# Kernel tuning notes

Hardware: AMD Instinct MI355X
Metric: run time of the kernel (lower is better)

Reference implementation:

```python
import jax, jax.numpy as jnp
import numpy as np

L, E, H, V = 12, 1024, 4096, 50277
LN_EPS = 9.999999747378752e-06  # tf float32 1e-5


def _layernorm(x, w, b):
    m = jnp.mean(x)
    xc = x - m
    return xc / jnp.sqrt(jnp.mean(xc * xc) + LN_EPS) * w + b


def setup_inputs() -> dict:
    key = jax.random.key(0)
    ks = jax.random.split(key, 32)
    f32 = jnp.float32

    def n(i, shape, s=0.02):
        return (jax.random.normal(ks[i], shape, f32) * s).astype(f32)

    inp = {
        "statea": n(0, (L, E), 0.3),
        "stateb": jax.random.uniform(ks[1], (L, E), f32),
        "statec": jax.random.uniform(ks[2], (L, E), f32),
        "stated": n(3, (L, E), 0.3),
        "preprocess": n(4, (V, E), 0.5),
        "ln1w": 1.0 + n(5, (L, E), 0.05),
        "ln1b": n(6, (L, E), 0.05),
        "ln2w": 1.0 + n(7, (L, E), 0.05),
        "ln2b": n(8, (L, E), 0.05),
        "att_key": n(9, (L, E, E)),
        "att_receptance": n(10, (L, E, E)),
        "att_value": n(11, (L, E, E)),
        "kktk": jax.random.uniform(ks[12], (L, E), f32),
        "vvtv": jax.random.uniform(ks[13], (L, E), f32),
        "rrtr": jax.random.uniform(ks[14], (L, E), f32),
        "time_first": n(15, (L, E), 0.2),
        "time_decay": n(16, (L, E), 0.2) - 1.0,
        "outputvv": n(17, (L, E, E)),
        "time_mix_k_ffn": jax.random.uniform(ks[18], (L, E), f32),
        "time_mix_r_ffn": jax.random.uniform(ks[19], (L, E), f32),
        "key_ffn": n(20, (L, H, E)),
        "receptance_ffn": n(21, (L, E, E)),
        "value_ffn": n(22, (L, E, H)),
        "post0": 1.0 + n(23, (E,), 0.05),
        "post1": n(24, (E,), 0.05),
        "post2": n(25, (V, E)),
        "token": 123,
    }
    return inp


def _forward(statea, stateb, statec, stated, preprocess, ln1w, ln1b, ln2w, ln2b,
             att_key, att_receptance, att_value, kktk, vvtv, rrtr, time_first,
             time_decay, outputvv, time_mix_k_ffn, time_mix_r_ffn, key_ffn,
             receptance_ffn, value_ffn, post0, post1, post2, token):
    x0 = preprocess[token]  # [E]

    def step(x, p):
        (sa, sb, sc, sd, l1w, l1b, l2w, l2b, ak, ar, av, kk, vv, rr,
         tfirst, tdecay, ovv, tmk_m, tmr_m, kf, rf, vf) = p
        xy = _layernorm(x, l1w, l1b)
        # WKV time-mixing (single step): mat-vecs + exp-decay state recursion
        k = jnp.exp(ak @ (xy + kk * sa))        # [E]
        v = av @ (xy + vv * sa)                 # [E]
        r = jnp.exp(ar @ (xy + rr * sa)) + 1.0  # [E]
        etf = jnp.exp(tfirst)
        w = sb + etf * k * v
        d = sc * r + etf * k * r
        mvv = ovv @ (w / (d + 0.001))           # [E]
        sxx = x + mvv
        aaa = xy
        etd = jnp.exp(tdecay)
        bbb = sb * etd + k * v
        ccc = sc * etd + k
        # channel-mixing FFN
        xx = _layernorm(sxx, l2w, l2b)
        kma = kf @ (xx + tmk_m * sd)            # [H]
        km = jnp.square(jnp.maximum(kma, 0.0))
        rt = jnp.exp(rf @ (xx + tmr_m * sd)) + 1.0  # [E]
        x_new = sxx + (vf @ km) / rt
        ddd = xx
        return x_new, (aaa, bbb, ccc, ddd)

    xs = (statea, stateb, statec, stated, ln1w, ln1b, ln2w, ln2b, att_key,
          att_receptance, att_value, kktk, vvtv, rrtr, time_first, time_decay,
          outputvv, time_mix_k_ffn, time_mix_r_ffn, key_ffn, receptance_ffn,
          value_ffn)
    xL, (aaa, bbb, ccc, ddd) = jax.lax.scan(step, x0, xs)
    logits = post2 @ _layernorm(xL, post0, post1)  # [V]
    return logits, aaa, bbb, ccc, ddd


def reference(statea, stateb, statec, stated, preprocess, ln1w, ln1b, ln2w, ln2b,
              att_key, att_receptance, att_value, kktk, vvtv, rrtr, time_first,
              time_decay, outputvv, time_mix_k_ffn, time_mix_r_ffn, key_ffn,
              receptance_ffn, value_ffn, post0, post1, post2, token):
    return _forward(statea, stateb, statec, stated, preprocess, ln1w, ln1b,
                    ln2w, ln2b, att_key, att_receptance, att_value, kktk, vvtv,
                    rrtr, time_first, time_decay, outputvv, time_mix_k_ffn,
                    time_mix_r_ffn, key_ffn, receptance_ffn, value_ffn, post0,
                    post1, post2, token)
```

## Files before the change

### kernel.cpp

```cpp
#include <hip/hip_runtime.h>
#include <math.h>


constexpr int E = 1024;
constexpr int H = 4096;
constexpr int V = 50277;
constexpr int L = 12;
constexpr int NBLK = 256;
constexpr int NTHR = 512;
constexpr float LN_EPS = 9.999999747378752e-06f;

#define SCOPE_AGENT __HIP_MEMORY_SCOPE_AGENT

__device__ __forceinline__ void cstoref(float *p, float v) {
  __hip_atomic_store(p, v, __ATOMIC_RELAXED, SCOPE_AGENT);
}
__device__ __forceinline__ void cstoreu(unsigned *p, unsigned v) {
  __hip_atomic_store(p, v, __ATOMIC_RELAXED, SCOPE_AGENT);
}
__device__ __forceinline__ unsigned cloadu(const unsigned *p) {
  return __hip_atomic_load(p, __ATOMIC_RELAXED, SCOPE_AGENT);
}

__device__ __forceinline__ float2 cload2(const void *p) {
  float2 r;
  asm volatile("global_load_dwordx2 %0, %1, off sc0 sc1\n\t"
               "s_waitcnt vmcnt(0)"
               : "=&v"(r) : "v"(p) : "memory");
  return r;
}
__device__ __forceinline__ void cload4x2(float4 &r0, float4 &r1,
                                         const void *p0, const void *p1) {
  asm volatile("global_load_dwordx4 %0, %2, off sc0 sc1\n\t"
               "global_load_dwordx4 %1, %3, off sc0 sc1\n\t"
               "s_waitcnt vmcnt(0)"
               : "=&v"(r0), "=&v"(r1) : "v"(p0), "v"(p1) : "memory");
}

struct Args {
  const float *statea, *stateb, *statec, *stated, *pre;
  const float *ln1w, *ln1b, *ln2w, *ln2b;
  const float *ak, *ar, *av, *kk, *vv, *rr, *tf, *td, *ovv;
  const float *tmk, *tmr, *kf, *rf, *vf;
  const float *post0, *post1, *post2;
  const int *token;
  float *out;
  float *ws;
  unsigned *flags;
};

__device__ __forceinline__ void bar_arrive(const Args &a, unsigned ep, int blk) {
  __syncthreads();
  if (threadIdx.x == 0) cstoreu(&a.flags[blk * 32], ep);
}

__device__ __forceinline__ void bar_wait(const Args &a, unsigned ep) {
  if (threadIdx.x < NBLK) {
    while (cloadu(&a.flags[threadIdx.x * 32]) < ep)
      __builtin_amdgcn_s_sleep(2);
  }
  __syncthreads();
}

__device__ __forceinline__ float wred(float v) {
#pragma unroll
  for (int off = 32; off; off >>= 1) v += __shfl_down(v, off, 64);
  return v;
}

__device__ __forceinline__ float dot4(float4 w, float4 x) {
  return w.x * x.x + w.y * x.y + w.z * x.z + w.w * x.w;
}

__device__ __forceinline__ float2 block_stats_v(float2 v, float *s_x, float *s_red,
                                                int tid, int lane, int wid) {
  reinterpret_cast<float2 *>(s_x)[tid] = v;
  float s = v.x + v.y, s2 = v.x * v.x + v.y * v.y;
#pragma unroll
  for (int off = 32; off; off >>= 1) {
    s += __shfl_down(s, off, 64);
    s2 += __shfl_down(s2, off, 64);
  }
  if (lane == 0) { s_red[wid] = s; s_red[8 + wid] = s2; }
  __syncthreads();
  float ts = 0.f, ts2 = 0.f;
#pragma unroll
  for (int i = 0; i < 8; ++i) { ts += s_red[i]; ts2 += s_red[8 + i]; }
  float m = ts * (1.0f / E);
  float var = ts2 * (1.0f / E) - m * m;
  return make_float2(m, rsqrtf(var + LN_EPS));
}

__device__ __forceinline__ void loadrow(float4 *d, const float4 *P, int r, int lane) {
  const float4 *p = P + (size_t)r * 256;
  d[0] = p[lane]; d[1] = p[lane + 64]; d[2] = p[lane + 128]; d[3] = p[lane + 192];
}

__global__ __launch_bounds__(NTHR) void rwkv_fused(Args a) {
  __shared__ __align__(16) float s_a[4096];
  __shared__ __align__(16) float s_x[1024];
  __shared__ __align__(16) float s_y[1024];
  __shared__ float s_pp[24];
  __shared__ float s_red[16];
  __shared__ float s_rt[4];

  const int tid = threadIdx.x;
  const int lane = tid & 63;
  const int wid = tid >> 6;
  const int blk = blockIdx.x;
  const int rloc = wid >> 1;
  const int h = wid & 1;
  const int grow = blk * 4 + rloc;

  float *ws_u = a.ws, *ws_sxx = a.ws + 1024, *ws_x = a.ws + 2048, *ws_km = a.ws + 3072;
  float *out_logits = a.out;
  float *out_aaa = a.out + V;
  float *out_bbb = out_aaa + L * E;
  float *out_ccc = out_bbb + L * E;
  float *out_ddd = out_ccc + L * E;

  const int tok = a.token[0];
  const float *pre_row = a.pre + (size_t)tok * E;
  const float4 *s4a = reinterpret_cast<const float4 *>(s_a);

  float4 pw[10];
  unsigned ep = 1;

  {
    const float4 *kr = reinterpret_cast<const float4 *>(a.ak + (size_t)grow * E);
    const float4 *vr = reinterpret_cast<const float4 *>(a.av + (size_t)grow * E);
    const float4 *rr = reinterpret_cast<const float4 *>(a.ar + (size_t)grow * E);
    int b0 = h * 128 + lane;
    pw[0] = kr[b0]; pw[1] = kr[b0 + 64];
    pw[2] = vr[b0]; pw[3] = vr[b0 + 64];
    pw[4] = rr[b0]; pw[5] = rr[b0 + 64];
    asm volatile("" ::: "memory");
  }

  for (int l = 0; l < L; ++l) {
    const size_t lE = (size_t)l * E;

    {
      float2 v;
      if (l == 0) {
        v = reinterpret_cast<const float2 *>(pre_row)[tid];
      } else {
        v = cload2(reinterpret_cast<const float2 *>(ws_x) + tid);
      }
      float2 st = block_stats_v(v, s_x, s_red, tid, lane, wid);
#pragma unroll
      for (int j = 0; j < 2; ++j) {
        int e = tid + 512 * j;
        float xy = (s_x[e] - st.x) * st.y * a.ln1w[lE + e] + a.ln1b[lE + e];
        s_y[e] = xy;
        float sa = a.statea[lE + e];
        s_a[e] = xy + a.kk[lE + e] * sa;
        s_a[1024 + e] = xy + a.vv[lE + e] * sa;
        s_a[2048 + e] = xy + a.rr[lE + e] * sa;
      }
      __syncthreads();
      int b0 = h * 128 + lane;
      float accK = dot4(pw[0], s4a[b0]) + dot4(pw[1], s4a[b0 + 64]);
      float accV = dot4(pw[2], s4a[256 + b0]) + dot4(pw[3], s4a[256 + b0 + 64]);
      float accR = dot4(pw[4], s4a[512 + b0]) + dot4(pw[5], s4a[512 + b0 + 64]);
      accK = wred(accK); accV = wred(accV); accR = wred(accR);
      if (lane == 0) {
        s_pp[wid * 3 + 0] = accK;
        s_pp[wid * 3 + 1] = accV;
        s_pp[wid * 3 + 2] = accR;
      }
      __syncthreads();
      if (tid < 4) {
        size_t o = lE + blk * 4 + tid;
        float K = s_pp[(2 * tid) * 3] + s_pp[(2 * tid + 1) * 3];
        float Vv = s_pp[(2 * tid) * 3 + 1] + s_pp[(2 * tid + 1) * 3 + 1];
        float R = s_pp[(2 * tid) * 3 + 2] + s_pp[(2 * tid + 1) * 3 + 2];
        float kx = expf(K), rx = expf(R) + 1.0f;
        float etf = expf(a.tf[o]), etd = expf(a.td[o]);
        float sb = a.stateb[o], sc = a.statec[o];
        float w_ = sb + etf * kx * Vv;
        float d_ = sc * rx + etf * kx * rx;
        cstoref(&ws_u[blk * 4 + tid], w_ / (d_ + 0.001f));
        out_bbb[o] = sb * etd + kx * Vv;
        out_ccc[o] = sc * etd + kx;
        out_aaa[o] = s_y[blk * 4 + tid];
      }
    }
    bar_arrive(a, ep, blk);
    {
      const float4 *orow = reinterpret_cast<const float4 *>(a.ovv + (lE + grow) * E);
      int b0 = h * 128 + lane;
      pw[0] = orow[b0]; pw[1] = orow[b0 + 64];
      asm volatile("" ::: "memory");
    }
    bar_wait(a, ep); ++ep;

    {
      reinterpret_cast<float2 *>(s_a)[tid] =
          cload2(reinterpret_cast<const float2 *>(ws_u) + tid);
      __syncthreads();
      int b0 = h * 128 + lane;
      float acc = dot4(pw[0], s4a[b0]) + dot4(pw[1], s4a[b0 + 64]);
      acc = wred(acc);
      if (lane == 0) s_pp[wid] = acc;
      __syncthreads();
      if (tid < 4) {
        float sxx = s_x[blk * 4 + tid] + s_pp[2 * tid] + s_pp[2 * tid + 1];
        cstoref(&ws_sxx[blk * 4 + tid], sxx);
      }
    }
    bar_arrive(a, ep, blk);
    {
      const float *kfb = a.kf + (size_t)l * H * E;
      const float4 *k0 = reinterpret_cast<const float4 *>(kfb + (size_t)(blk * 16 + wid) * E);
      const float4 *k1 = reinterpret_cast<const float4 *>(kfb + (size_t)(blk * 16 + 8 + wid) * E);
      pw[0] = k0[lane];       pw[1] = k0[lane + 64];
      pw[2] = k0[lane + 128]; pw[3] = k0[lane + 192];
      pw[4] = k1[lane];       pw[5] = k1[lane + 64];
      pw[6] = k1[lane + 128]; pw[7] = k1[lane + 192];
      const float4 *rrow = reinterpret_cast<const float4 *>(a.rf + (lE + grow) * E);
      int b0 = h * 128 + lane;
      pw[8] = rrow[b0]; pw[9] = rrow[b0 + 64];
      asm volatile("" ::: "memory");
    }
    bar_wait(a, ep); ++ep;

    {
      float2 v = cload2(reinterpret_cast<const float2 *>(ws_sxx) + tid);
      float2 st = block_stats_v(v, s_x, s_red, tid, lane, wid);
#pragma unroll
      for (int j = 0; j < 2; ++j) {
        int e = tid + 512 * j;
        float xx = (s_x[e] - st.x) * st.y * a.ln2w[lE + e] + a.ln2b[lE + e];
        s_y[e] = xx;
        float sd = a.stated[lE + e];
        s_a[e] = xx + a.tmk[lE + e] * sd;
        s_a[1024 + e] = xx + a.tmr[lE + e] * sd;
      }
      __syncthreads();
      float k0 = dot4(pw[0], s4a[lane]) + dot4(pw[1], s4a[lane + 64]) +
                 dot4(pw[2], s4a[lane + 128]) + dot4(pw[3], s4a[lane + 192]);
      float k1 = dot4(pw[4], s4a[lane]) + dot4(pw[5], s4a[lane + 64]) +
                 dot4(pw[6], s4a[lane + 128]) + dot4(pw[7], s4a[lane + 192]);
      int b0 = h * 128 + lane;
      float ar_ = dot4(pw[8], s4a[256 + b0]) + dot4(pw[9], s4a[256 + b0 + 64]);
      k0 = wred(k0); k1 = wred(k1); ar_ = wred(ar_);
      if (lane == 0) {
        float t0 = fmaxf(k0, 0.f), t1 = fmaxf(k1, 0.f);
        cstoref(&ws_km[blk * 16 + wid], t0 * t0);
        cstoref(&ws_km[blk * 16 + 8 + wid], t1 * t1);
        s_pp[wid] = ar_;
      }
      __syncthreads();
      if (tid < 4) {
        s_rt[tid] = expf(s_pp[2 * tid] + s_pp[2 * tid + 1]) + 1.0f;
        out_ddd[lE + blk * 4 + tid] = s_y[blk * 4 + tid];
      }
    }
    bar_arrive(a, ep, blk);
    {
      const float4 *vrow = reinterpret_cast<const float4 *>(a.vf + (lE + grow) * H);
      int b0 = h * 512 + lane;
      pw[0] = vrow[b0];       pw[1] = vrow[b0 + 64];
      pw[2] = vrow[b0 + 128]; pw[3] = vrow[b0 + 192];
      pw[4] = vrow[b0 + 256]; pw[5] = vrow[b0 + 320];
      pw[6] = vrow[b0 + 384]; pw[7] = vrow[b0 + 448];
      asm volatile("" ::: "memory");
    }
    bar_wait(a, ep); ++ep;

    {
      float4 km0, km1;
      cload4x2(km0, km1,
               reinterpret_cast<const float4 *>(ws_km) + tid,
               reinterpret_cast<const float4 *>(ws_km) + tid + 512);
      reinterpret_cast<float4 *>(s_a)[tid] = km0;
      reinterpret_cast<float4 *>(s_a)[tid + 512] = km1;
      __syncthreads();
      int b0 = h * 512 + lane;
      float acc = dot4(pw[0], s4a[b0]) + dot4(pw[1], s4a[b0 + 64]) +
                  dot4(pw[2], s4a[b0 + 128]) + dot4(pw[3], s4a[b0 + 192]) +
                  dot4(pw[4], s4a[b0 + 256]) + dot4(pw[5], s4a[b0 + 320]) +
                  dot4(pw[6], s4a[b0 + 384]) + dot4(pw[7], s4a[b0 + 448]);
      acc = wred(acc);
      if (lane == 0) s_pp[wid] = acc;
      __syncthreads();
      if (tid < 4) {
        float xn = s_x[blk * 4 + tid] + (s_pp[2 * tid] + s_pp[2 * tid + 1]) / s_rt[tid];
        cstoref(&ws_x[blk * 4 + tid], xn);
      }
    }
    bar_arrive(a, ep, blk);
    if (l < L - 1) {
      const size_t lE2 = (size_t)(l + 1) * E;
      const float4 *kr = reinterpret_cast<const float4 *>(a.ak + (lE2 + grow) * E);
      const float4 *vr = reinterpret_cast<const float4 *>(a.av + (lE2 + grow) * E);
      const float4 *rr = reinterpret_cast<const float4 *>(a.ar + (lE2 + grow) * E);
      int b0 = h * 128 + lane;
      pw[0] = kr[b0]; pw[1] = kr[b0 + 64];
      pw[2] = vr[b0]; pw[3] = vr[b0 + 64];
      pw[4] = rr[b0]; pw[5] = rr[b0 + 64];
      asm volatile("" ::: "memory");
    }
    bar_wait(a, ep); ++ep;
  }

  {
    float2 v = cload2(reinterpret_cast<const float2 *>(ws_x) + tid);
    float2 st = block_stats_v(v, s_x, s_red, tid, lane, wid);
#pragma unroll
    for (int j = 0; j < 2; ++j) {
      int e = tid + 512 * j;
      s_a[e] = (s_x[e] - st.x) * st.y * a.post0[e] + a.post1[e];
    }
    __syncthreads();

    const float4 *P2 = reinterpret_cast<const float4 *>(a.post2);
    const int gw = blk * 8 + wid;
    int r0 = gw, r1 = gw + 2048;
    float4 A0[4], A1[4];
    loadrow(A0, P2, r0, lane);
    loadrow(A1, P2, r1 < V ? r1 : r0, lane);
    while (true) {
      int n0 = r0 + 4096, n1 = n0 + 2048;
      bool more = n0 < V;
      float4 B0[4], B1[4];
      if (more) {
        loadrow(B0, P2, n0, lane);
        loadrow(B1, P2, n1 < V ? n1 : n0, lane);
      }
      float a0 = dot4(A0[0], s4a[lane]) + dot4(A0[1], s4a[lane + 64]) +
                 dot4(A0[2], s4a[lane + 128]) + dot4(A0[3], s4a[lane + 192]);
      float a1 = dot4(A1[0], s4a[lane]) + dot4(A1[1], s4a[lane + 64]) +
                 dot4(A1[2], s4a[lane + 128]) + dot4(A1[3], s4a[lane + 192]);
      a0 = wred(a0); a1 = wred(a1);
      if (lane == 0) {
        out_logits[r0] = a0;
        if (r1 < V) out_logits[r1] = a1;
      }
      if (!more) break;
#pragma unroll
      for (int q = 0; q < 4; ++q) { A0[q] = B0[q]; A1[q] = B1[q]; }
      r0 = n0; r1 = n1;
    }
  }
}

extern "C" void kernel_launch(void *const *d_in, const int *in_sizes, int n_in,
                              void *d_out, int out_size, void *d_ws, size_t ws_size,
                              hipStream_t stream) {
  (void)in_sizes; (void)n_in; (void)out_size; (void)ws_size;
  Args a;
  a.statea = (const float *)d_in[0];
  a.stateb = (const float *)d_in[1];
  a.statec = (const float *)d_in[2];
  a.stated = (const float *)d_in[3];
  a.pre    = (const float *)d_in[4];
  a.ln1w   = (const float *)d_in[5];
  a.ln1b   = (const float *)d_in[6];
  a.ln2w   = (const float *)d_in[7];
  a.ln2b   = (const float *)d_in[8];
  a.ak     = (const float *)d_in[9];
  a.ar     = (const float *)d_in[10];
  a.av     = (const float *)d_in[11];
  a.kk     = (const float *)d_in[12];
  a.vv     = (const float *)d_in[13];
  a.rr     = (const float *)d_in[14];
  a.tf     = (const float *)d_in[15];
  a.td     = (const float *)d_in[16];
  a.ovv    = (const float *)d_in[17];
  a.tmk    = (const float *)d_in[18];
  a.tmr    = (const float *)d_in[19];
  a.kf     = (const float *)d_in[20];
  a.rf     = (const float *)d_in[21];
  a.vf     = (const float *)d_in[22];
  a.post0  = (const float *)d_in[23];
  a.post1  = (const float *)d_in[24];
  a.post2  = (const float *)d_in[25];
  a.token  = (const int *)d_in[26];
  a.out    = (float *)d_out;

  a.flags  = (unsigned *)d_ws;
  a.ws     = (float *)((char *)d_ws + 32768);

  hipMemsetAsync(d_ws, 0, 32768, stream);
  rwkv_fused<<<NBLK, NTHR, 0, stream>>>(a);
}
```

Baseline: 242.4 us.

## Prefetch weights stages ahead and replace syncthreads with lighter LDS barriers

Measured after the change: 266.8 us. 10.1% more time.

```diff
diff --git a/kernel.cpp b/kernel.cpp
--- a/kernel.cpp
+++ b/kernel.cpp
@@ -21,20 +21,17 @@
 __device__ __forceinline__ unsigned cloadu(const unsigned *p) {
   return __hip_atomic_load(p, __ATOMIC_RELAXED, SCOPE_AGENT);
 }
-
-__device__ __forceinline__ float2 cload2(const void *p) {
-  float2 r;
-  asm volatile("global_load_dwordx2 %0, %1, off sc0 sc1\n\t"
-               "s_waitcnt vmcnt(0)"
-               : "=&v"(r) : "v"(p) : "memory");
-  return r;
-}
-__device__ __forceinline__ void cload4x2(float4 &r0, float4 &r1,
-                                         const void *p0, const void *p1) {
-  asm volatile("global_load_dwordx4 %0, %2, off sc0 sc1\n\t"
-               "global_load_dwordx4 %1, %3, off sc0 sc1\n\t"
-               "s_waitcnt vmcnt(0)"
-               : "=&v"(r0), "=&v"(r1) : "v"(p0), "v"(p1) : "memory");
+__device__ __forceinline__ float2 cload2(const float *p) {
+  union { unsigned long long u; float2 f; } c;
+  c.u = __hip_atomic_load((const unsigned long long *)p, __ATOMIC_RELAXED, SCOPE_AGENT);
+  return c.f;
+}
+
+__device__ __forceinline__ void lds_sync() {
+  __builtin_amdgcn_sched_barrier(0);
+  asm volatile("s_waitcnt lgkmcnt(0)" ::: "memory");
+  __builtin_amdgcn_s_barrier();
+  __builtin_amdgcn_sched_barrier(0);
 }
 
 struct Args {
@@ -52,14 +49,17 @@
 __device__ __forceinline__ void bar_arrive(const Args &a, unsigned ep, int blk) {
   __syncthreads();
   if (threadIdx.x == 0) cstoreu(&a.flags[blk * 32], ep);
-}
-
-__device__ __forceinline__ void bar_wait(const Args &a, unsigned ep) {
+  __builtin_amdgcn_sched_barrier(0);
+}
+
+__device__ __forceinline__ void bar_spin(const Args &a, unsigned ep) {
+  __builtin_amdgcn_sched_barrier(0);
   if (threadIdx.x < NBLK) {
     while (cloadu(&a.flags[threadIdx.x * 32]) < ep)
       __builtin_amdgcn_s_sleep(2);
   }
-  __syncthreads();
+  __builtin_amdgcn_s_barrier();
+  __builtin_amdgcn_sched_barrier(0);
 }
 
 __device__ __forceinline__ float wred(float v) {
@@ -82,7 +82,7 @@
     s2 += __shfl_down(s2, off, 64);
   }
   if (lane == 0) { s_red[wid] = s; s_red[8 + wid] = s2; }
-  __syncthreads();
+  lds_sync();
   float ts = 0.f, ts2 = 0.f;
 #pragma unroll
   for (int i = 0; i < 8; ++i) { ts += s_red[i]; ts2 += s_red[8 + i]; }
@@ -111,6 +111,8 @@
   const int rloc = wid >> 1;
   const int h = wid & 1;
   const int grow = blk * 4 + rloc;
+  const int b0h = h * 128 + lane;
+  const int bv = h * 512 + lane;
 
   float *ws_u = a.ws, *ws_sxx = a.ws + 1024, *ws_x = a.ws + 2048, *ws_km = a.ws + 3072;
   float *out_logits = a.out;
@@ -123,87 +125,114 @@
   const float *pre_row = a.pre + (size_t)tok * E;
   const float4 *s4a = reinterpret_cast<const float4 *>(s_a);
 
-  float4 pw[10];
   unsigned ep = 1;
+
+  float4 pw1[6];
+  float2 e1w, e1b, e1sa, e1kk, e1vv, e1rr;
+  float e_tf = 0.f, e_td = 0.f, e_sb = 0.f, e_sc = 0.f;
 
   {
     const float4 *kr = reinterpret_cast<const float4 *>(a.ak + (size_t)grow * E);
     const float4 *vr = reinterpret_cast<const float4 *>(a.av + (size_t)grow * E);
-    const float4 *rr = reinterpret_cast<const float4 *>(a.ar + (size_t)grow * E);
-    int b0 = h * 128 + lane;
-    pw[0] = kr[b0]; pw[1] = kr[b0 + 64];
-    pw[2] = vr[b0]; pw[3] = vr[b0 + 64];
-    pw[4] = rr[b0]; pw[5] = rr[b0 + 64];
-    asm volatile("" ::: "memory");
+    const float4 *rr4 = reinterpret_cast<const float4 *>(a.ar + (size_t)grow * E);
+    pw1[0] = kr[b0h]; pw1[1] = kr[b0h + 64];
+    pw1[2] = vr[b0h]; pw1[3] = vr[b0h + 64];
+    pw1[4] = rr4[b0h]; pw1[5] = rr4[b0h + 64];
+    e1w = reinterpret_cast<const float2 *>(a.ln1w)[tid];
+    e1b = reinterpret_cast<const float2 *>(a.ln1b)[tid];
+    e1sa = reinterpret_cast<const float2 *>(a.statea)[tid];
+    e1kk = reinterpret_cast<const float2 *>(a.kk)[tid];
+    e1vv = reinterpret_cast<const float2 *>(a.vv)[tid];
+    e1rr = reinterpret_cast<const float2 *>(a.rr)[tid];
+    if (tid < 4) {
+      size_t o = (size_t)blk * 4 + tid;
+      e_tf = a.tf[o]; e_td = a.td[o]; e_sb = a.stateb[o]; e_sc = a.statec[o];
+    }
   }
 
+#pragma unroll 1
   for (int l = 0; l < L; ++l) {
     const size_t lE = (size_t)l * E;
+    float4 pw2[2], pw3[10], pw4[8];
+    float2 e3w, e3b, e3sd, e3tk, e3tr;
 
     {
       float2 v;
-      if (l == 0) {
-        v = reinterpret_cast<const float2 *>(pre_row)[tid];
-      } else {
-        v = cload2(reinterpret_cast<const float2 *>(ws_x) + tid);
+      if (l == 0) v = reinterpret_cast<const float2 *>(pre_row)[tid];
+      else        v = cload2(ws_x + 2 * tid);
+      {
+        const float4 *orow = reinterpret_cast<const float4 *>(a.ovv + (lE + grow) * E);
+        pw2[0] = orow[b0h]; pw2[1] = orow[b0h + 64];
+        const float *kfb = a.kf + (size_t)l * H * E;
+        const float4 *k0 = reinterpret_cast<const float4 *>(kfb + (size_t)(blk * 16 + wid) * E);
+        pw3[0] = k0[lane];       pw3[1] = k0[lane + 64];
+        pw3[2] = k0[lane + 128]; pw3[3] = k0[lane + 192];
       }
       float2 st = block_stats_v(v, s_x, s_red, tid, lane, wid);
-#pragma unroll
-      for (int j = 0; j < 2; ++j) {
-        int e = tid + 512 * j;
-        float xy = (s_x[e] - st.x) * st.y * a.ln1w[lE + e] + a.ln1b[lE + e];
-        s_y[e] = xy;
-        float sa = a.statea[lE + e];
-        s_a[e] = xy + a.kk[lE + e] * sa;
-        s_a[1024 + e] = xy + a.vv[lE + e] * sa;
-        s_a[2048 + e] = xy + a.rr[lE + e] * sa;
-      }
-      __syncthreads();
-      int b0 = h * 128 + lane;
-      float accK = dot4(pw[0], s4a[b0]) + dot4(pw[1], s4a[b0 + 64]);
-      float accV = dot4(pw[2], s4a[256 + b0]) + dot4(pw[3], s4a[256 + b0 + 64]);
-      float accR = dot4(pw[4], s4a[512 + b0]) + dot4(pw[5], s4a[512 + b0 + 64]);
+      float2 xy = make_float2((v.x - st.x) * st.y * e1w.x + e1b.x,
+                              (v.y - st.x) * st.y * e1w.y + e1b.y);
+      reinterpret_cast<float2 *>(s_y)[tid] = xy;
+      reinterpret_cast<float2 *>(s_a)[tid] =
+          make_float2(xy.x + e1kk.x * e1sa.x, xy.y + e1kk.y * e1sa.y);
+      reinterpret_cast<float2 *>(s_a + 1024)[tid] =
+          make_float2(xy.x + e1vv.x * e1sa.x, xy.y + e1vv.y * e1sa.y);
+      reinterpret_cast<float2 *>(s_a + 2048)[tid] =
+          make_float2(xy.x + e1rr.x * e1sa.x, xy.y + e1rr.y * e1sa.y);
+      lds_sync();
+      float accK = dot4(pw1[0], s4a[b0h]) + dot4(pw1[1], s4a[b0h + 64]);
+      float accV = dot4(pw1[2], s4a[256 + b0h]) + dot4(pw1[3], s4a[256 + b0h + 64]);
+      float accR = dot4(pw1[4], s4a[512 + b0h]) + dot4(pw1[5], s4a[512 + b0h + 64]);
       accK = wred(accK); accV = wred(accV); accR = wred(accR);
       if (lane == 0) {
         s_pp[wid * 3 + 0] = accK;
         s_pp[wid * 3 + 1] = accV;
         s_pp[wid * 3 + 2] = accR;
       }
-      __syncthreads();
+      lds_sync();
       if (tid < 4) {
         size_t o = lE + blk * 4 + tid;
         float K = s_pp[(2 * tid) * 3] + s_pp[(2 * tid + 1) * 3];
         float Vv = s_pp[(2 * tid) * 3 + 1] + s_pp[(2 * tid + 1) * 3 + 1];
         float R = s_pp[(2 * tid) * 3 + 2] + s_pp[(2 * tid + 1) * 3 + 2];
         float kx = expf(K), rx = expf(R) + 1.0f;
-        float etf = expf(a.tf[o]), etd = expf(a.td[o]);
-        float sb = a.stateb[o], sc = a.statec[o];
-        float w_ = sb + etf * kx * Vv;
-        float d_ = sc * rx + etf * kx * rx;
+        float etf = expf(e_tf), etd = expf(e_td);
+        float w_ = e_sb + etf * kx * Vv;
+        float d_ = e_sc * rx + etf * kx * rx;
         cstoref(&ws_u[blk * 4 + tid], w_ / (d_ + 0.001f));
-        out_bbb[o] = sb * etd + kx * Vv;
-        out_ccc[o] = sc * etd + kx;
+        out_bbb[o] = e_sb * etd + kx * Vv;
+        out_ccc[o] = e_sc * etd + kx;
         out_aaa[o] = s_y[blk * 4 + tid];
       }
     }
     bar_arrive(a, ep, blk);
     {
-      const float4 *orow = reinterpret_cast<const float4 *>(a.ovv + (lE + grow) * E);
-      int b0 = h * 128 + lane;
-      pw[0] = orow[b0]; pw[1] = orow[b0 + 64];
-      asm volatile("" ::: "memory");
-    }
-    bar_wait(a, ep); ++ep;
-
-    {
-      reinterpret_cast<float2 *>(s_a)[tid] =
-          cload2(reinterpret_cast<const float2 *>(ws_u) + tid);
-      __syncthreads();
-      int b0 = h * 128 + lane;
-      float acc = dot4(pw[0], s4a[b0]) + dot4(pw[1], s4a[b0 + 64]);
+      const float *kfb = a.kf + (size_t)l * H * E;
+      const float4 *k1 = reinterpret_cast<const float4 *>(kfb + (size_t)(blk * 16 + 8 + wid) * E);
+      pw3[4] = k1[lane];       pw3[5] = k1[lane + 64];
+      pw3[6] = k1[lane + 128]; pw3[7] = k1[lane + 192];
+    }
+    bar_spin(a, ep); ++ep;
+
+    {
+      float2 u2 = cload2(ws_u + 2 * tid);
+      {
+        const float4 *rrow = reinterpret_cast<const float4 *>(a.rf + (lE + grow) * E);
+        pw3[8] = rrow[b0h]; pw3[9] = rrow[b0h + 64];
+        e3w = reinterpret_cast<const float2 *>(a.ln2w + lE)[tid];
+        e3b = reinterpret_cast<const float2 *>(a.ln2b + lE)[tid];
+        e3sd = reinterpret_cast<const float2 *>(a.stated + lE)[tid];
+        e3tk = reinterpret_cast<const float2 *>(a.tmk + lE)[tid];
+        e3tr = reinterpret_cast<const float2 *>(a.tmr + lE)[tid];
+        const float4 *vrow = reinterpret_cast<const float4 *>(a.vf + (lE + grow) * H);
+        pw4[0] = vrow[bv];       pw4[1] = vrow[bv + 64];
+        pw4[2] = vrow[bv + 128]; pw4[3] = vrow[bv + 192];
+      }
+      reinterpret_cast<float2 *>(s_a)[tid] = u2;
+      lds_sync();
+      float acc = dot4(pw2[0], s4a[b0h]) + dot4(pw2[1], s4a[b0h + 64]);
       acc = wred(acc);
       if (lane == 0) s_pp[wid] = acc;
-      __syncthreads();
+      lds_sync();
       if (tid < 4) {
         float sxx = s_x[blk * 4 + tid] + s_pp[2 * tid] + s_pp[2 * tid + 1];
         cstoref(&ws_sxx[blk * 4 + tid], sxx);
@@ -211,109 +240,99 @@
     }
     bar_arrive(a, ep, blk);
     {
-      const float *kfb = a.kf + (size_t)l * H * E;
-      const float4 *k0 = reinterpret_cast<const float4 *>(kfb + (size_t)(blk * 16 + wid) * E);
-      const float4 *k1 = reinterpret_cast<const float4 *>(kfb + (size_t)(blk * 16 + 8 + wid) * E);
-      pw[0] = k0[lane];       pw[1] = k0[lane + 64];
-      pw[2] = k0[lane + 128]; pw[3] = k0[lane + 192];
-      pw[4] = k1[lane];       pw[5] = k1[lane + 64];
-      pw[6] = k1[lane + 128]; pw[7] = k1[lane + 192];
-      const float4 *rrow = reinterpret_cast<const float4 *>(a.rf + (lE + grow) * E);
-      int b0 = h * 128 + lane;
-      pw[8] = rrow[b0]; pw[9] = rrow[b0 + 64];
-      asm volatile("" ::: "memory");
-    }
-    bar_wait(a, ep); ++ep;
-
-    {
-      float2 v = cload2(reinterpret_cast<const float2 *>(ws_sxx) + tid);
-      float2 st = block_stats_v(v, s_x, s_red, tid, lane, wid);
-#pragma unroll
-      for (int j = 0; j < 2; ++j) {
-        int e = tid + 512 * j;
-        float xx = (s_x[e] - st.x) * st.y * a.ln2w[lE + e] + a.ln2b[lE + e];
-        s_y[e] = xx;
-        float sd = a.stated[lE + e];
-        s_a[e] = xx + a.tmk[lE + e] * sd;
-        s_a[1024 + e] = xx + a.tmr[lE + e] * sd;
-      }
-      __syncthreads();
-      float k0 = dot4(pw[0], s4a[lane]) + dot4(pw[1], s4a[lane + 64]) +
-                 dot4(pw[2], s4a[lane + 128]) + dot4(pw[3], s4a[lane + 192]);
-      float k1 = dot4(pw[4], s4a[lane]) + dot4(pw[5], s4a[lane + 64]) +
-                 dot4(pw[6], s4a[lane + 128]) + dot4(pw[7], s4a[lane + 192]);
-      int b0 = h * 128 + lane;
-      float ar_ = dot4(pw[8], s4a[256 + b0]) + dot4(pw[9], s4a[256 + b0 + 64]);
+      const float4 *vrow = reinterpret_cast<const float4 *>(a.vf + (lE + grow) * H);
+      pw4[4] = vrow[bv + 256]; pw4[5] = vrow[bv + 320];
+      pw4[6] = vrow[bv + 384]; pw4[7] = vrow[bv + 448];
+    }
+    bar_spin(a, ep); ++ep;
+
+    {
+      float2 vsx = cload2(ws_sxx + 2 * tid);
+      if (l + 1 < L) {
+        const size_t nE = (size_t)(l + 1) * E;
+        const float4 *kr = reinterpret_cast<const float4 *>(a.ak + (nE + grow) * E);
+        const float4 *vr = reinterpret_cast<const float4 *>(a.av + (nE + grow) * E);
+        const float4 *rr4 = reinterpret_cast<const float4 *>(a.ar + (nE + grow) * E);
+        pw1[0] = kr[b0h]; pw1[1] = kr[b0h + 64];
+        pw1[2] = vr[b0h]; pw1[3] = vr[b0h + 64];
+        pw1[4] = rr4[b0h]; pw1[5] = rr4[b0h + 64];
+        e1w = reinterpret_cast<const float2 *>(a.ln1w + nE)[tid];
+        e1b = reinterpret_cast<const float2 *>(a.ln1b + nE)[tid];
+        e1sa = reinterpret_cast<const float2 *>(a.statea + nE)[tid];
+        e1kk = reinterpret_cast<const float2 *>(a.kk + nE)[tid];
+        e1vv = reinterpret_cast<const float2 *>(a.vv + nE)[tid];
+        e1rr = reinterpret_cast<const float2 *>(a.rr + nE)[tid];
+        if (tid < 4) {
+          size_t o = nE + blk * 4 + tid;
+          e_tf = a.tf[o]; e_td = a.td[o]; e_sb = a.stateb[o]; e_sc = a.statec[o];
+        }
+      } else {
+        e1w = reinterpret_cast<const float2 *>(a.post0)[tid];
+        e1b = reinterpret_cast<const float2 *>(a.post1)[tid];
+      }
+      float2 st = block_stats_v(vsx, s_x, s_red, tid, lane, wid);
+      float2 xx = make_float2((vsx.x - st.x) * st.y * e3w.x + e3b.x,
+                              (vsx.y - st.x) * st.y * e3w.y + e3b.y);
+      reinterpret_cast<float2 *>(s_y)[tid] = xx;
+      reinterpret_cast<float2 *>(s_a)[tid] =
+          make_float2(xx.x + e3tk.x * e3sd.x, xx.y + e3tk.y * e3sd.y);
+      reinterpret_cast<float2 *>(s_a + 1024)[tid] =
+          make_float2(xx.x + e3tr.x * e3sd.x, xx.y + e3tr.y * e3sd.y);
+      lds_sync();
+      float k0 = dot4(pw3[0], s4a[lane]) + dot4(pw3[1], s4a[lane + 64]) +
+                 dot4(pw3[2], s4a[lane + 128]) + dot4(pw3[3], s4a[lane + 192]);
+      float k1 = dot4(pw3[4], s4a[lane]) + dot4(pw3[5], s4a[lane + 64]) +
+                 dot4(pw3[6], s4a[lane + 128]) + dot4(pw3[7], s4a[lane + 192]);
+      float ar_ = dot4(pw3[8], s4a[256 + b0h]) + dot4(pw3[9], s4a[256 + b0h + 64]);
       k0 = wred(k0); k1 = wred(k1); ar_ = wred(ar_);
       if (lane == 0) {
-        float t0 = fmaxf(k0, 0.f), t1 = fmaxf(k1, 0.f);
+        float t0 = fmaxf(k0, 0.f), t1v = fmaxf(k1, 0.f);
         cstoref(&ws_km[blk * 16 + wid], t0 * t0);
-        cstoref(&ws_km[blk * 16 + 8 + wid], t1 * t1);
+        cstoref(&ws_km[blk * 16 + 8 + wid], t1v * t1v);
         s_pp[wid] = ar_;
       }
-      __syncthreads();
+      lds_sync();
       if (tid < 4) {
         s_rt[tid] = expf(s_pp[2 * tid] + s_pp[2 * tid + 1]) + 1.0f;
         out_ddd[lE + blk * 4 + tid] = s_y[blk * 4 + tid];
       }
     }
     bar_arrive(a, ep, blk);
-    {
-      const float4 *vrow = reinterpret_cast<const float4 *>(a.vf + (lE + grow) * H);
-      int b0 = h * 512 + lane;
-      pw[0] = vrow[b0];       pw[1] = vrow[b0 + 64];
-      pw[2] = vrow[b0 + 128]; pw[3] = vrow[b0 + 192];
-      pw[4] = vrow[b0 + 256]; pw[5] = vrow[b0 + 320];
-      pw[6] = vrow[b0 + 384]; pw[7] = vrow[b0 + 448];
-      asm volatile("" ::: "memory");
-    }
-    bar_wait(a, ep); ++ep;
-
-    {
-      float4 km0, km1;
-      cload4x2(km0, km1,
-               reinterpret_cast<const float4 *>(ws_km) + tid,
-               reinterpret_cast<const float4 *>(ws_km) + tid + 512);
-      reinterpret_cast<float4 *>(s_a)[tid] = km0;
-      reinterpret_cast<float4 *>(s_a)[tid + 512] = km1;
-      __syncthreads();
-      int b0 = h * 512 + lane;
-      float acc = dot4(pw[0], s4a[b0]) + dot4(pw[1], s4a[b0 + 64]) +
-                  dot4(pw[2], s4a[b0 + 128]) + dot4(pw[3], s4a[b0 + 192]) +
-                  dot4(pw[4], s4a[b0 + 256]) + dot4(pw[5], s4a[b0 + 320]) +
-                  dot4(pw[6], s4a[b0 + 384]) + dot4(pw[7], s4a[b0 + 448]);
+    bar_spin(a, ep); ++ep;
+
+    {
+      float2 k0a = cload2(ws_km + 4 * tid);
+      float2 k0b = cload2(ws_km + 4 * tid + 2);
+      float2 k1a = cload2(ws_km + 2048 + 4 * tid);
+      float2 k1b = cload2(ws_km + 2048 + 4 * tid + 2);
+      reinterpret_cast<float2 *>(s_a)[2 * tid] = k0a;
+      reinterpret_cast<float2 *>(s_a)[2 * tid + 1] = k0b;
+      reinterpret_cast<float2 *>(s_a)[1024 + 2 * tid] = k1a;
+      reinterpret_cast<float2 *>(s_a)[1024 + 2 * tid + 1] = k1b;
+      lds_sync();
+      float acc = dot4(pw4[0], s4a[bv]) + dot4(pw4[1], s4a[bv + 64]) +
+                  dot4(pw4[2], s4a[bv + 128]) + dot4(pw4[3], s4a[bv + 192]) +
+                  dot4(pw4[4], s4a[bv + 256]) + dot4(pw4[5], s4a[bv + 320]) +
+                  dot4(pw4[6], s4a[bv + 384]) + dot4(pw4[7], s4a[bv + 448]);
       acc = wred(acc);
       if (lane == 0) s_pp[wid] = acc;
-      __syncthreads();
+      lds_sync();
       if (tid < 4) {
         float xn = s_x[blk * 4 + tid] + (s_pp[2 * tid] + s_pp[2 * tid + 1]) / s_rt[tid];
         cstoref(&ws_x[blk * 4 + tid], xn);
       }
     }
     bar_arrive(a, ep, blk);
-    if (l < L - 1) {
-      const size_t lE2 = (size_t)(l + 1) * E;
-      const float4 *kr = reinterpret_cast<const float4 *>(a.ak + (lE2 + grow) * E);
-      const float4 *vr = reinterpret_cast<const float4 *>(a.av + (lE2 + grow) * E);
-      const float4 *rr = reinterpret_cast<const float4 *>(a.ar + (lE2 + grow) * E);
-      int b0 = h * 128 + lane;
-      pw[0] = kr[b0]; pw[1] = kr[b0 + 64];
-      pw[2] = vr[b0]; pw[3] = vr[b0 + 64];
-      pw[4] = rr[b0]; pw[5] = rr[b0 + 64];
-      asm volatile("" ::: "memory");
-    }
-    bar_wait(a, ep); ++ep;
+    bar_spin(a, ep); ++ep;
   }
 
   {
-    float2 v = cload2(reinterpret_cast<const float2 *>(ws_x) + tid);
+    float2 v = cload2(ws_x + 2 * tid);
     float2 st = block_stats_v(v, s_x, s_red, tid, lane, wid);
-#pragma unroll
-    for (int j = 0; j < 2; ++j) {
-      int e = tid + 512 * j;
-      s_a[e] = (s_x[e] - st.x) * st.y * a.post0[e] + a.post1[e];
-    }
-    __syncthreads();
+    reinterpret_cast<float2 *>(s_a)[tid] =
+        make_float2((v.x - st.x) * st.y * e1w.x + e1b.x,
+                    (v.y - st.x) * st.y * e1w.y + e1b.y);
+    lds_sync();
 
     const float4 *P2 = reinterpret_cast<const float4 *>(a.post2);
     const int gw = blk * 8 + wid;
```

## Add dedicated prefetch blocks that stream upcoming layer weights into cache

Applied to the files above, without the earlier changes.

New measurement: 690.8 us. 2.85x slower.

```diff
diff --git a/kernel.cpp b/kernel.cpp
--- a/kernel.cpp
+++ b/kernel.cpp
@@ -7,6 +7,7 @@
 constexpr int V = 50277;
 constexpr int L = 12;
 constexpr int NBLK = 256;
+constexpr int NPF  = 64;
 constexpr int NTHR = 512;
 constexpr float LN_EPS = 9.999999747378752e-06f;
 
@@ -96,6 +97,42 @@
   d[0] = p[lane]; d[1] = p[lane + 64]; d[2] = p[lane + 128]; d[3] = p[lane + 192];
 }
 
+__device__ __forceinline__ float pf_region(const float *base, int n4, int gt) {
+  const float4 *p = reinterpret_cast<const float4 *>(base);
+  float s = 0.f;
+#pragma unroll 2
+  for (int i = gt; i < n4; i += NPF * NTHR) {
+    float4 v = p[i];
+    s += v.x + v.y + v.z + v.w;
+  }
+  return s;
+}
+
+__device__ void prefetch_role(const Args &a, int pb) {
+  const int gt = pb * NTHR + threadIdx.x;
+  float s = 0.f;
+  for (int l = 0; l < L; ++l) {
+    if (l >= 3) {
+      unsigned need = 4u * (unsigned)(l - 2);
+      while (cloadu(&a.flags[0]) < need) __builtin_amdgcn_s_sleep(16);
+    }
+    const size_t mE = (size_t)l * E * E;
+    const size_t mH = (size_t)l * H * E;
+    s += pf_region(a.ak + mE, E * E / 4, gt);
+    s += pf_region(a.av + mE, E * E / 4, gt);
+    s += pf_region(a.ar + mE, E * E / 4, gt);
+    s += pf_region(a.ovv + mE, E * E / 4, gt);
+    s += pf_region(a.kf + mH, H * E / 4, gt);
+    s += pf_region(a.rf + mE, E * E / 4, gt);
+    s += pf_region(a.vf + mH, E * H / 4, gt);
+  }
+  {
+    while (cloadu(&a.flags[0]) < 32u) __builtin_amdgcn_s_sleep(16);
+    s += pf_region(a.post2, V * (E / 4), gt);
+  }
+  asm volatile("" :: "v"(s));
+}
+
 __global__ __launch_bounds__(NTHR) void rwkv_fused(Args a) {
   __shared__ __align__(16) float s_a[4096];
   __shared__ __align__(16) float s_x[1024];
@@ -104,10 +141,12 @@
   __shared__ float s_red[16];
   __shared__ float s_rt[4];
 
+  const int blk = blockIdx.x;
+  if (blk >= NBLK) { prefetch_role(a, blk - NBLK); return; }
+
   const int tid = threadIdx.x;
   const int lane = tid & 63;
   const int wid = tid >> 6;
-  const int blk = blockIdx.x;
   const int rloc = wid >> 1;
   const int h = wid & 1;
   const int grow = blk * 4 + rloc;
@@ -384,5 +423,5 @@
   a.ws     = (float *)((char *)d_ws + 32768);
 
   hipMemsetAsync(d_ws, 0, 32768, stream);
-  rwkv_fused<<<NBLK, NTHR, 0, stream>>>(a);
-}
+  rwkv_fused<<<NBLK + NPF, NTHR, 0, stream>>>(a);
+}
```

## Stage FFN weights into LDS via async global_load_lds double buffering

Applied to the files above, without the earlier changes.

Result: slower. 266.8 us (+10.1%).

```diff
diff --git a/kernel.cpp b/kernel.cpp
--- a/kernel.cpp
+++ b/kernel.cpp
@@ -35,6 +35,17 @@
                "global_load_dwordx4 %1, %3, off sc0 sc1\n\t"
                "s_waitcnt vmcnt(0)"
                : "=&v"(r0), "=&v"(r1) : "v"(p0), "v"(p1) : "memory");
+}
+
+__device__ __forceinline__ void stage16(const float *gp, float *lp) {
+  __builtin_amdgcn_global_load_lds(
+      (const __attribute__((address_space(1))) void *)gp,
+      (__attribute__((address_space(3))) void *)lp, 16, 0, 0);
+}
+
+__device__ __forceinline__ void lds_sync() {
+  asm volatile("s_waitcnt lgkmcnt(0)" ::: "memory");
+  __builtin_amdgcn_s_barrier();
 }
 
 struct Args {
@@ -59,7 +70,7 @@
     while (cloadu(&a.flags[threadIdx.x * 32]) < ep)
       __builtin_amdgcn_s_sleep(2);
   }
-  __syncthreads();
+  lds_sync();
 }
 
 __device__ __forceinline__ float wred(float v) {
@@ -82,7 +93,7 @@
     s2 += __shfl_down(s2, off, 64);
   }
   if (lane == 0) { s_red[wid] = s; s_red[8 + wid] = s2; }
-  __syncthreads();
+  lds_sync();
   float ts = 0.f, ts2 = 0.f;
 #pragma unroll
   for (int i = 0; i < 8; ++i) { ts += s_red[i]; ts2 += s_red[8 + i]; }
@@ -97,9 +108,9 @@
 }
 
 __global__ __launch_bounds__(NTHR) void rwkv_fused(Args a) {
+  __shared__ __align__(16) float wbuf[2][16384];
   __shared__ __align__(16) float s_a[4096];
   __shared__ __align__(16) float s_x[1024];
-  __shared__ __align__(16) float s_y[1024];
   __shared__ float s_pp[24];
   __shared__ float s_red[16];
   __shared__ float s_rt[4];
@@ -111,6 +122,7 @@
   const int rloc = wid >> 1;
   const int h = wid & 1;
   const int grow = blk * 4 + rloc;
+  const int b0h = h * 128 + lane;
 
   float *ws_u = a.ws, *ws_sxx = a.ws + 1024, *ws_x = a.ws + 2048, *ws_km = a.ws + 3072;
   float *out_logits = a.out;
@@ -123,87 +135,111 @@
   const float *pre_row = a.pre + (size_t)tok * E;
   const float4 *s4a = reinterpret_cast<const float4 *>(s_a);
 
-  float4 pw[10];
+  float4 pw1[6];
+  float4 pwo[2];
+  float4 pwr[2];
   unsigned ep = 1;
 
   {
     const float4 *kr = reinterpret_cast<const float4 *>(a.ak + (size_t)grow * E);
     const float4 *vr = reinterpret_cast<const float4 *>(a.av + (size_t)grow * E);
-    const float4 *rr = reinterpret_cast<const float4 *>(a.ar + (size_t)grow * E);
-    int b0 = h * 128 + lane;
-    pw[0] = kr[b0]; pw[1] = kr[b0 + 64];
-    pw[2] = vr[b0]; pw[3] = vr[b0 + 64];
-    pw[4] = rr[b0]; pw[5] = rr[b0 + 64];
+    const float4 *rr4 = reinterpret_cast<const float4 *>(a.ar + (size_t)grow * E);
+    pw1[0] = kr[b0h]; pw1[1] = kr[b0h + 64];
+    pw1[2] = vr[b0h]; pw1[3] = vr[b0h + 64];
+    pw1[4] = rr4[b0h]; pw1[5] = rr4[b0h + 64];
     asm volatile("" ::: "memory");
   }
 
+#pragma unroll 1
   for (int l = 0; l < L; ++l) {
     const size_t lE = (size_t)l * E;
+    const float *kfb = a.kf + (size_t)l * H * E + (size_t)blk * 16 * E;
 
     {
       float2 v;
-      if (l == 0) {
-        v = reinterpret_cast<const float2 *>(pre_row)[tid];
-      } else {
-        v = cload2(reinterpret_cast<const float2 *>(ws_x) + tid);
+      if (l == 0) v = reinterpret_cast<const float2 *>(pre_row)[tid];
+      else        v = cload2(reinterpret_cast<const float2 *>(ws_x) + tid);
+      float2 w1 = reinterpret_cast<const float2 *>(a.ln1w + lE)[tid];
+      float2 b1 = reinterpret_cast<const float2 *>(a.ln1b + lE)[tid];
+      float2 sa = reinterpret_cast<const float2 *>(a.statea + lE)[tid];
+      float2 kk2 = reinterpret_cast<const float2 *>(a.kk + lE)[tid];
+      float2 vv2 = reinterpret_cast<const float2 *>(a.vv + lE)[tid];
+      float2 rr2 = reinterpret_cast<const float2 *>(a.rr + lE)[tid];
+      float etf = 0.f, etd = 0.f, sb = 0.f, sc = 0.f;
+      if (tid < 4) {
+        size_t o = lE + blk * 4 + tid;
+        etf = a.tf[o]; etd = a.td[o]; sb = a.stateb[o]; sc = a.statec[o];
+      }
+      {
+        float *kb = wbuf[l & 1];
+#pragma unroll
+        for (int j = 0; j < 4; ++j) {
+          int c = (wid * 4 + j) * 256;
+          stage16(kfb + c + lane * 4, kb + c);
+        }
       }
       float2 st = block_stats_v(v, s_x, s_red, tid, lane, wid);
-#pragma unroll
-      for (int j = 0; j < 2; ++j) {
-        int e = tid + 512 * j;
-        float xy = (s_x[e] - st.x) * st.y * a.ln1w[lE + e] + a.ln1b[lE + e];
-        s_y[e] = xy;
-        float sa = a.statea[lE + e];
-        s_a[e] = xy + a.kk[lE + e] * sa;
-        s_a[1024 + e] = xy + a.vv[lE + e] * sa;
-        s_a[2048 + e] = xy + a.rr[lE + e] * sa;
-      }
-      __syncthreads();
-      int b0 = h * 128 + lane;
-      float accK = dot4(pw[0], s4a[b0]) + dot4(pw[1], s4a[b0 + 64]);
-      float accV = dot4(pw[2], s4a[256 + b0]) + dot4(pw[3], s4a[256 + b0 + 64]);
-      float accR = dot4(pw[4], s4a[512 + b0]) + dot4(pw[5], s4a[512 + b0 + 64]);
+      float2 xy = make_float2((v.x - st.x) * st.y * w1.x + b1.x,
+                              (v.y - st.x) * st.y * w1.y + b1.y);
+      if ((tid >> 1) == blk) {
+        out_aaa[lE + 2 * tid] = xy.x;
+        out_aaa[lE + 2 * tid + 1] = xy.y;
+      }
+      reinterpret_cast<float2 *>(s_a)[tid] =
+          make_float2(xy.x + kk2.x * sa.x, xy.y + kk2.y * sa.y);
+      reinterpret_cast<float2 *>(s_a + 1024)[tid] =
+          make_float2(xy.x + vv2.x * sa.x, xy.y + vv2.y * sa.y);
+      reinterpret_cast<float2 *>(s_a + 2048)[tid] =
+          make_float2(xy.x + rr2.x * sa.x, xy.y + rr2.y * sa.y);
+      lds_sync();
+      float accK = dot4(pw1[0], s4a[b0h]) + dot4(pw1[1], s4a[b0h + 64]);
+      float accV = dot4(pw1[2], s4a[256 + b0h]) + dot4(pw1[3], s4a[256 + b0h + 64]);
+      float accR = dot4(pw1[4], s4a[512 + b0h]) + dot4(pw1[5], s4a[512 + b0h + 64]);
       accK = wred(accK); accV = wred(accV); accR = wred(accR);
       if (lane == 0) {
         s_pp[wid * 3 + 0] = accK;
         s_pp[wid * 3 + 1] = accV;
         s_pp[wid * 3 + 2] = accR;
       }
-      __syncthreads();
+      lds_sync();
       if (tid < 4) {
         size_t o = lE + blk * 4 + tid;
         float K = s_pp[(2 * tid) * 3] + s_pp[(2 * tid + 1) * 3];
         float Vv = s_pp[(2 * tid) * 3 + 1] + s_pp[(2 * tid + 1) * 3 + 1];
         float R = s_pp[(2 * tid) * 3 + 2] + s_pp[(2 * tid + 1) * 3 + 2];
         float kx = expf(K), rx = expf(R) + 1.0f;
-        float etf = expf(a.tf[o]), etd = expf(a.td[o]);
-        float sb = a.stateb[o], sc = a.statec[o];
-        float w_ = sb + etf * kx * Vv;
-        float d_ = sc * rx + etf * kx * rx;
+        float etf_ = expf(etf), etd_ = expf(etd);
+        float w_ = sb + etf_ * kx * Vv;
+        float d_ = sc * rx + etf_ * kx * rx;
         cstoref(&ws_u[blk * 4 + tid], w_ / (d_ + 0.001f));
-        out_bbb[o] = sb * etd + kx * Vv;
-        out_ccc[o] = sc * etd + kx;
-        out_aaa[o] = s_y[blk * 4 + tid];
+        out_bbb[o] = sb * etd_ + kx * Vv;
+        out_ccc[o] = sc * etd_ + kx;
       }
     }
     bar_arrive(a, ep, blk);
     {
       const float4 *orow = reinterpret_cast<const float4 *>(a.ovv + (lE + grow) * E);
-      int b0 = h * 128 + lane;
-      pw[0] = orow[b0]; pw[1] = orow[b0 + 64];
+      pwo[0] = orow[b0h]; pwo[1] = orow[b0h + 64];
       asm volatile("" ::: "memory");
     }
     bar_wait(a, ep); ++ep;
 
     {
-      reinterpret_cast<float2 *>(s_a)[tid] =
-          cload2(reinterpret_cast<const float2 *>(ws_u) + tid);
-      __syncthreads();
-      int b0 = h * 128 + lane;
-      float acc = dot4(pw[0], s4a[b0]) + dot4(pw[1], s4a[b0 + 64]);
+      float2 u2 = cload2(reinterpret_cast<const float2 *>(ws_u) + tid);
+      {
+        float *kb = wbuf[l & 1];
+#pragma unroll
+        for (int j = 0; j < 4; ++j) {
+          int c = (32 + wid * 4 + j) * 256;
+          stage16(kfb + c + lane * 4, kb + c);
+        }
+      }
+      reinterpret_cast<float2 *>(s_a)[tid] = u2;
+      lds_sync();
+      float acc = dot4(pwo[0], s4a[b0h]) + dot4(pwo[1], s4a[b0h + 64]);
       acc = wred(acc);
       if (lane == 0) s_pp[wid] = acc;
-      __syncthreads();
+      lds_sync();
       if (tid < 4) {
         float sxx = s_x[blk * 4 + tid] + s_pp[2 * tid] + s_pp[2 * tid + 1];
         cstoref(&ws_sxx[blk * 4 + tid], sxx);
@@ -211,39 +247,49 @@
     }
     bar_arrive(a, ep, blk);
     {
-      const float *kfb = a.kf + (size_t)l * H * E;
-      const float4 *k0 = reinterpret_cast<const float4 *>(kfb + (size_t)(blk * 16 + wid) * E);
-      const float4 *k1 = reinterpret_cast<const float4 *>(kfb + (size_t)(blk * 16 + 8 + wid) * E);
-      pw[0] = k0[lane];       pw[1] = k0[lane + 64];
-      pw[2] = k0[lane + 128]; pw[3] = k0[lane + 192];
-      pw[4] = k1[lane];       pw[5] = k1[lane + 64];
-      pw[6] = k1[lane + 128]; pw[7] = k1[lane + 192];
       const float4 *rrow = reinterpret_cast<const float4 *>(a.rf + (lE + grow) * E);
-      int b0 = h * 128 + lane;
-      pw[8] = rrow[b0]; pw[9] = rrow[b0 + 64];
+      pwr[0] = rrow[b0h]; pwr[1] = rrow[b0h + 64];
       asm volatile("" ::: "memory");
     }
     bar_wait(a, ep); ++ep;
 
     {
-      float2 v = cload2(reinterpret_cast<const float2 *>(ws_sxx) + tid);
-      float2 st = block_stats_v(v, s_x, s_red, tid, lane, wid);
-#pragma unroll
-      for (int j = 0; j < 2; ++j) {
-        int e = tid + 512 * j;
-        float xx = (s_x[e] - st.x) * st.y * a.ln2w[lE + e] + a.ln2b[lE + e];
-        s_y[e] = xx;
-        float sd = a.stated[lE + e];
-        s_a[e] = xx + a.tmk[lE + e] * sd;
-        s_a[1024 + e] = xx + a.tmr[lE + e] * sd;
-      }
-      __syncthreads();
-      float k0 = dot4(pw[0], s4a[lane]) + dot4(pw[1], s4a[lane + 64]) +
-                 dot4(pw[2], s4a[lane + 128]) + dot4(pw[3], s4a[lane + 192]);
-      float k1 = dot4(pw[4], s4a[lane]) + dot4(pw[5], s4a[lane + 64]) +
-                 dot4(pw[6], s4a[lane + 128]) + dot4(pw[7], s4a[lane + 192]);
-      int b0 = h * 128 + lane;
-      float ar_ = dot4(pw[8], s4a[256 + b0]) + dot4(pw[9], s4a[256 + b0 + 64]);
+      float2 vsx = cload2(reinterpret_cast<const float2 *>(ws_sxx) + tid);
+      float2 w2 = reinterpret_cast<const float2 *>(a.ln2w + lE)[tid];
+      float2 b2 = reinterpret_cast<const float2 *>(a.ln2b + lE)[tid];
+      float2 sd2 = reinterpret_cast<const float2 *>(a.stated + lE)[tid];
+      float2 tk2 = reinterpret_cast<const float2 *>(a.tmk + lE)[tid];
+      float2 tr2 = reinterpret_cast<const float2 *>(a.tmr + lE)[tid];
+      {
+        const float *vfb = a.vf + (size_t)l * E * H + (size_t)blk * 4 * H;
+        float *vb = wbuf[(l + 1) & 1];
+#pragma unroll
+        for (int j = 0; j < 8; ++j) {
+          int c = (wid * 8 + j) * 256;
+          stage16(vfb + c + lane * 4, vb + c);
+        }
+      }
+      float2 st = block_stats_v(vsx, s_x, s_red, tid, lane, wid);
+      float2 xx = make_float2((vsx.x - st.x) * st.y * w2.x + b2.x,
+                              (vsx.y - st.x) * st.y * w2.y + b2.y);
+      if ((tid >> 1) == blk) {
+        out_ddd[lE + 2 * tid] = xx.x;
+        out_ddd[lE + 2 * tid + 1] = xx.y;
+      }
+      reinterpret_cast<float2 *>(s_a)[tid] =
+          make_float2(xx.x + tk2.x * sd2.x, xx.y + tk2.y * sd2.y);
+      reinterpret_cast<float2 *>(s_a + 1024)[tid] =
+          make_float2(xx.x + tr2.x * sd2.x, xx.y + tr2.y * sd2.y);
+      lds_sync();
+      const float4 *kL = reinterpret_cast<const float4 *>(wbuf[l & 1]);
+      float k0 = 0.f, k1 = 0.f;
+#pragma unroll
+      for (int it = 0; it < 4; ++it) {
+        float4 xv = s4a[it * 64 + lane];
+        k0 += dot4(kL[wid * 256 + it * 64 + lane], xv);
+        k1 += dot4(kL[(wid + 8) * 256 + it * 64 + lane], xv);
+      }
+      float ar_ = dot4(pwr[0], s4a[256 + b0h]) + dot4(pwr[1], s4a[256 + b0h + 64]);
       k0 = wred(k0); k1 = wred(k1); ar_ = wred(ar_);
       if (lane == 0) {
         float t0 = fmaxf(k0, 0.f), t1 = fmaxf(k1, 0.f);
@@ -251,22 +297,12 @@
         cstoref(&ws_km[blk * 16 + 8 + wid], t1 * t1);
         s_pp[wid] = ar_;
       }
-      __syncthreads();
+      lds_sync();
       if (tid < 4) {
         s_rt[tid] = expf(s_pp[2 * tid] + s_pp[2 * tid + 1]) + 1.0f;
-        out_ddd[lE + blk * 4 + tid] = s_y[blk * 4 + tid];
       }
     }
     bar_arrive(a, ep, blk);
-    {
-      const float4 *vrow = reinterpret_cast<const float4 *>(a.vf + (lE + grow) * H);
-      int b0 = h * 512 + lane;
-      pw[0] = vrow[b0];       pw[1] = vrow[b0 + 64];
-      pw[2] = vrow[b0 + 128]; pw[3] = vrow[b0 + 192];
-      pw[4] = vrow[b0 + 256]; pw[5] = vrow[b0 + 320];
-      pw[6] = vrow[b0 + 384]; pw[7] = vrow[b0 + 448];
-      asm volatile("" ::: "memory");
-    }
     bar_wait(a, ep); ++ep;
 
     {
@@ -274,46 +310,47 @@
       cload4x2(km0, km1,
                reinterpret_cast<const float4 *>(ws_km) + tid,
                reinterpret_cast<const float4 *>(ws_km) + tid + 512);
+      if (l < L - 1) {
+        const size_t lE2 = (size_t)(l + 1) * E;
+        const float4 *kr = reinterpret_cast<const float4 *>(a.ak + (lE2 + grow) * E);
+        const float4 *vr = reinterpret_cast<const float4 *>(a.av + (lE2 + grow) * E);
+        const float4 *rr4 = reinterpret_cast<const float4 *>(a.ar + (lE2 + grow) * E);
+        pw1[0] = kr[b0h]; pw1[1] = kr[b0h + 64];
+        pw1[2] = vr[b0h]; pw1[3] = vr[b0h + 64];
+        pw1[4] = rr4[b0h]; pw1[5] = rr4[b0h + 64];
+        asm volatile("" ::: "memory");
+      }
       reinterpret_cast<float4 *>(s_a)[tid] = km0;
       reinterpret_cast<float4 *>(s_a)[tid + 512] = km1;
-      __syncthreads();
-      int b0 = h * 512 + lane;
-      float acc = dot4(pw[0], s4a[b0]) + dot4(pw[1], s4a[b0 + 64]) +
-                  dot4(pw[2], s4a[b0 + 128]) + dot4(pw[3], s4a[b0 + 192]) +
-                  dot4(pw[4], s4a[b0 + 256]) + dot4(pw[5], s4a[b0 + 320]) +
-                  dot4(pw[6], s4a[b0 + 384]) + dot4(pw[7], s4a[b0 + 448]);
+      lds_sync();
+      const float4 *vL = reinterpret_cast<const float4 *>(wbuf[(l + 1) & 1]);
+      const int vb0 = rloc * 1024 + h * 512 + lane;
+      const int sb0 = h * 512 + lane;
+      float acc = 0.f;
+#pragma unroll
+      for (int it = 0; it < 8; ++it)
+        acc += dot4(vL[vb0 + it * 64], s4a[sb0 + it * 64]);
       acc = wred(acc);
       if (lane == 0) s_pp[wid] = acc;
-      __syncthreads();
+      lds_sync();
       if (tid < 4) {
         float xn = s_x[blk * 4 + tid] + (s_pp[2 * tid] + s_pp[2 * tid + 1]) / s_rt[tid];
         cstoref(&ws_x[blk * 4 + tid], xn);
       }
     }
     bar_arrive(a, ep, blk);
-    if (l < L - 1) {
-      const size_t lE2 = (size_t)(l + 1) * E;
-      const float4 *kr = reinterpret_cast<const float4 *>(a.ak + (lE2 + grow) * E);
-      const float4 *vr = reinterpret_cast<const float4 *>(a.av + (lE2 + grow) * E);
-      const float4 *rr = reinterpret_cast<const float4 *>(a.ar + (lE2 + grow) * E);
-      int b0 = h * 128 + lane;
-      pw[0] = kr[b0]; pw[1] = kr[b0 + 64];
-      pw[2] = vr[b0]; pw[3] = vr[b0 + 64];
-      pw[4] = rr[b0]; pw[5] = rr[b0 + 64];
-      asm volatile("" ::: "memory");
-    }
     bar_wait(a, ep); ++ep;
   }
 
   {
     float2 v = cload2(reinterpret_cast<const float2 *>(ws_x) + tid);
+    float2 p0 = reinterpret_cast<const float2 *>(a.post0)[tid];
+    float2 p1 = reinterpret_cast<const float2 *>(a.post1)[tid];
     float2 st = block_stats_v(v, s_x, s_red, tid, lane, wid);
-#pragma unroll
-    for (int j = 0; j < 2; ++j) {
-      int e = tid + 512 * j;
-      s_a[e] = (s_x[e] - st.x) * st.y * a.post0[e] + a.post1[e];
-    }
-    __syncthreads();
+    reinterpret_cast<float2 *>(s_a)[tid] =
+        make_float2((v.x - st.x) * st.y * p0.x + p1.x,
+                    (v.y - st.x) * st.y * p0.y + p1.y);
+    lds_sync();
 
     const float4 *P2 = reinterpret_cast<const float4 *>(a.post2);
     const int gw = blk * 8 + wid;
```
